# Optimization experiments

Measured on AMD Instinct MI355X. Metric: run time of the kernel, lower is better.

## Reference

```python
import jax, jax.numpy as jnp
import numpy as np

B, N, D, R = 4, 50000, 64, 500
E_PER = 62500
E = B * E_PER


def _build_edges():
    rng = np.random.default_rng(0)
    idx = np.repeat(np.arange(B), E_PER)
    vi = rng.integers(0, N, E)
    vj = rng.integers(0, N, E)
    order = np.lexsort((vj, vi, idx))
    idx, vi, vj = idx[order], vi[order], vj[order]
    rel = rng.integers(0, R, E)
    key_vi = idx.astype(np.int64) * N + vi
    _, idx_vi = np.unique(key_vi, return_inverse=True)  # sorted -> nondecreasing segment ids
    key_vj = idx.astype(np.int64) * N + vj
    _, idx_vj = np.unique(key_vj, return_inverse=True)
    all_keys = np.concatenate([key_vi, key_vj])
    uniq_all, inv = np.unique(all_keys, return_inverse=True)
    e2vi, e2vj = inv[:E], inv[E:]
    sel = np.stack([idx, vi, vj, rel, idx_vi, idx_vj, e2vi, e2vj], axis=1).astype(np.int32)
    return sel, int(idx_vi.max() + 1), int(idx_vj.max() + 1), int(len(uniq_all))


def setup_inputs() -> dict:
    sel, n_vi_seg, n_vj_seg, n_visited = _build_edges()
    key = jax.random.key(0)
    ks = jax.random.split(key, 9)
    na = jax.random.uniform(ks[0], (B, N), jnp.float32) + 1e-6
    na = na / jnp.sum(na, axis=1, keepdims=True)
    return {
        'node_attention': na,
        'selected_edges': jnp.asarray(sel),
        'edges_y': jax.random.uniform(ks[1], (E,), jnp.float32, 0.1, 1.0),
        'hidden_con': jax.random.normal(ks[2], (n_visited, D), jnp.float32) * 0.1,
        'hidden_uncon': jax.random.normal(ks[3], (1, N, D), jnp.float32) * 0.1,
        'rel_emb': jax.random.normal(ks[4], (R, D), jnp.float32) * 0.1,
        'ws': jax.random.normal(ks[5], (8, D), jnp.float32) * (1.0 / np.sqrt(8.0)),
        'b': jax.random.normal(ks[6], (D,), jnp.float32) * 0.01,
        'out_w': jax.random.normal(ks[7], (D,), jnp.float32) * 0.3,
        'out_b': jax.random.normal(ks[8], (D,), jnp.float32) * 0.01,
        'n_vi_seg': n_vi_seg,
        'n_vj_seg': n_vj_seg,
    }


def reference(node_attention, selected_edges, edges_y, hidden_con, hidden_uncon,
              rel_emb, ws, b, out_w, out_b, n_vi_seg, n_vj_seg):
    idx, vi, vj = selected_edges[:, 0], selected_edges[:, 1], selected_edges[:, 2]
    rel, idx_vi, idx_vj = selected_edges[:, 3], selected_edges[:, 4], selected_edges[:, 5]
    e2vi, e2vj = selected_edges[:, 6], selected_edges[:, 7]

    # Node2Edge gathers
    hc_vi, hc_vj = hidden_con[e2vi], hidden_con[e2vj]        # [E, D]
    hu = hidden_uncon[0]                                     # hidden_uncon has batch 1
    hu_vi, hu_vj = hu[vi], hu[vj]                            # [E, D]
    re = rel_emb[rel]                                        # [E, D]

    # F layer: interact = [[0,3],[0,2,3],[0,4],[0,2,4],[1,3],[1,2,3],[1,4],[1,2,4]]
    terms = (hc_vi * hc_vj, hc_vi * re * hc_vj, hc_vi * hu_vj, hc_vi * re * hu_vj,
             hu_vi * hc_vj, hu_vi * re * hc_vj, hu_vi * hu_vj, hu_vi * re * hu_vj)
    f = b
    for k in range(8):
        f = f + ws[k] * terms[k]
    f = jax.nn.relu(f) * out_w + out_b                       # [E, D]
    logits = jnp.sum(f, axis=1)                              # [E]

    # NeighborSoftmax at='vi' (segment softmax)
    seg_max = jax.ops.segment_max(logits, idx_vi, num_segments=n_vi_seg)
    e = jnp.exp(logits - seg_max[idx_vi])
    es = jax.ops.segment_sum(e, idx_vi, num_segments=n_vi_seg)
    transition = e / es[idx_vi]

    # attention flow
    na_e = node_attention[idx, vi]
    ta = na_e * transition * edges_y

    # Aggregate at='vj', sum, then scatter into (B, n_nodes)
    aggr = jax.ops.segment_sum(ta, idx_vj, num_segments=n_vj_seg)
    seg_idx = jax.ops.segment_max(idx, idx_vj, num_segments=n_vj_seg)
    seg_vj = jax.ops.segment_max(vj, idx_vj, num_segments=n_vj_seg)
    Bn, Nn = node_attention.shape
    new_att = jnp.zeros((Bn, Nn), node_attention.dtype).at[seg_idx, seg_vj].add(aggr)
    return new_att / jnp.sum(new_att, axis=1, keepdims=True)
```

## Files before the change

### kernel.cpp

```cpp
#include <hip/hip_runtime.h>
#include <math.h>

#define D 64

__global__ __launch_bounds__(256) void k_logits(
    const int* __restrict__ sel, const float* __restrict__ hc,
    const float* __restrict__ hu, const float* __restrict__ re,
    const float* __restrict__ wsm, const float* __restrict__ bias,
    const float* __restrict__ out_w, const float* __restrict__ out_b,
    float* __restrict__ logits, int* __restrict__ seg_start,
    float* __restrict__ out, float* __restrict__ row_sum,
    int E, int BN, int Bn)
{
    const int tid = blockIdx.x * 256 + threadIdx.x;
    const int nthreads = gridDim.x * 256;

    for (int i = tid; i < BN; i += nthreads) out[i] = 0.f;
    if (tid < Bn) row_sum[tid] = 0.f;

    const int lane = threadIdx.x & 63;
    const int g    = lane >> 4;
    const int d16  = lane & 15;

    const float4* wsm4 = (const float4*)wsm;
    float4 W[8];
    #pragma unroll
    for (int k = 0; k < 8; ++k) W[k] = wsm4[k * 16 + d16];
    const float4 Bv = ((const float4*)bias)[d16];
    const float4 Ow = ((const float4*)out_w)[d16];
    const float4 Ob = ((const float4*)out_b)[d16];
    const float* Wf  = (const float*)W;
    const float* Bvf = (const float*)&Bv;
    const float* Owf = (const float*)&Ow;
    const float* Obf = (const float*)&Ob;

    const float4* hc4 = (const float4*)hc;
    const float4* hu4 = (const float4*)hu;
    const float4* re4 = (const float4*)re;

    const int wave   = tid >> 6;
    const int nwaves = nthreads >> 6;
    const int octs   = (E + 7) >> 3;

    int q = wave;
    if (q >= octs) return;

    int ec0 = min(q * 8 + g, E - 1);
    int ec1 = min(q * 8 + 4 + g, E - 1);
    int4 sA0 = *(const int4*)(sel + (size_t)ec0 * 8);
    int4 sB0 = *(const int4*)(sel + (size_t)ec0 * 8 + 4);
    int4 sA1 = *(const int4*)(sel + (size_t)ec1 * 8);
    int4 sB1 = *(const int4*)(sel + (size_t)ec1 * 8 + 4);

    for (; q < octs; q += nwaves) {
        const int e0 = q * 8 + g;
        const int e1 = q * 8 + 4 + g;
        const bool v0 = (e0 < E);
        const bool v1 = (e1 < E);

        const float4 a0  = hc4[(size_t)sB0.z * 16 + d16];
        const float4 c0  = hc4[(size_t)sB0.w * 16 + d16];
        const float4 ui0 = hu4[(size_t)sA0.y * 16 + d16];
        const float4 uj0 = hu4[(size_t)sA0.z * 16 + d16];
        const float4 r0  = re4[(size_t)sA0.w * 16 + d16];
        const float4 a1  = hc4[(size_t)sB1.z * 16 + d16];
        const float4 c1  = hc4[(size_t)sB1.w * 16 + d16];
        const float4 ui1 = hu4[(size_t)sA1.y * 16 + d16];
        const float4 uj1 = hu4[(size_t)sA1.z * 16 + d16];
        const float4 r1  = re4[(size_t)sA1.w * 16 + d16];

        const int qn = q + nwaves;
        int4 nA0, nB0, nA1, nB1;
        const bool more = (qn < octs);
        {
            const int pe0 = more ? min(qn * 8 + g, E - 1) : ec0;
            const int pe1 = more ? min(qn * 8 + 4 + g, E - 1) : ec1;
            nA0 = *(const int4*)(sel + (size_t)pe0 * 8);
            nB0 = *(const int4*)(sel + (size_t)pe0 * 8 + 4);
            nA1 = *(const int4*)(sel + (size_t)pe1 * 8);
            nB1 = *(const int4*)(sel + (size_t)pe1 * 8 + 4);
            ec0 = pe0; ec1 = pe1;
        }

        float acc0 = 0.f, acc1 = 0.f;
        {
            const float* ap = (const float*)&a0;  const float* cp = (const float*)&c0;
            const float* up = (const float*)&ui0; const float* vp = (const float*)&uj0;
            const float* rp = (const float*)&r0;
            #pragma unroll
            for (int k4 = 0; k4 < 4; ++k4) {
                const float hcvi = ap[k4], hcvj = cp[k4], huvi = up[k4], huvj = vp[k4], rr = rp[k4];
                const float p = hcvi * hcvj, qq = hcvi * huvj, ss = huvi * hcvj, uu = huvi * huvj;
                const float w01 = fmaf(rr, Wf[1*4+k4], Wf[0*4+k4]);
                const float w23 = fmaf(rr, Wf[3*4+k4], Wf[2*4+k4]);
                const float w45 = fmaf(rr, Wf[5*4+k4], Wf[4*4+k4]);
                const float w67 = fmaf(rr, Wf[7*4+k4], Wf[6*4+k4]);
                float f = fmaf(p, w01, Bvf[k4]);
                f = fmaf(qq, w23, f);
                f = fmaf(ss, w45, f);
                f = fmaf(uu, w67, f);
                acc0 += fmaf(fmaxf(f, 0.f), Owf[k4], Obf[k4]);
            }
        }
        {
            const float* ap = (const float*)&a1;  const float* cp = (const float*)&c1;
            const float* up = (const float*)&ui1; const float* vp = (const float*)&uj1;
            const float* rp = (const float*)&r1;
            #pragma unroll
            for (int k4 = 0; k4 < 4; ++k4) {
                const float hcvi = ap[k4], hcvj = cp[k4], huvi = up[k4], huvj = vp[k4], rr = rp[k4];
                const float p = hcvi * hcvj, qq = hcvi * huvj, ss = huvi * hcvj, uu = huvi * huvj;
                const float w01 = fmaf(rr, Wf[1*4+k4], Wf[0*4+k4]);
                const float w23 = fmaf(rr, Wf[3*4+k4], Wf[2*4+k4]);
                const float w45 = fmaf(rr, Wf[5*4+k4], Wf[4*4+k4]);
                const float w67 = fmaf(rr, Wf[7*4+k4], Wf[6*4+k4]);
                float f = fmaf(p, w01, Bvf[k4]);
                f = fmaf(qq, w23, f);
                f = fmaf(ss, w45, f);
                f = fmaf(uu, w67, f);
                acc1 += fmaf(fmaxf(f, 0.f), Owf[k4], Obf[k4]);
            }
        }

        #pragma unroll
        for (int off = 8; off > 0; off >>= 1) {
            acc0 += __shfl_xor(acc0, off, 64);
            acc1 += __shfl_xor(acc1, off, 64);
        }

        const int idxvi0 = sB0.x, idxvi1 = sB1.x;
        const int srcm16 = (lane >= 16) ? (lane - 16) : lane;
        const int p0w = __shfl(idxvi0, srcm16, 64);
        const int p1w = __shfl(idxvi1, srcm16, 64);
        const int p1b = __shfl(idxvi0, 48 + d16, 64);

        if (d16 == 0) {
            if (v0) {
                logits[e0] = acc0;
                int prev;
                if (e0 == 0)     prev = -1;
                else if (g == 0) prev = sel[(size_t)(e0 - 1) * 8 + 4];
                else             prev = p0w;
                if (idxvi0 != prev) seg_start[idxvi0] = e0;
                if (e0 == E - 1) seg_start[idxvi0 + 1] = E;
            }
            if (v1) {
                logits[e1] = acc1;
                const int prev = (g == 0) ? p1b : p1w;
                if (idxvi1 != prev) seg_start[idxvi1] = e1;
                if (e1 == E - 1) seg_start[idxvi1 + 1] = E;
            }
        }

        sA0 = nA0; sB0 = nB0; sA1 = nA1; sB1 = nB1;
    }
}

__global__ __launch_bounds__(256) void k_softmax_scatter(
    const int* __restrict__ sel, const float* __restrict__ logits,
    const int* __restrict__ seg_start, const float* __restrict__ na,
    const float* __restrict__ edges_y,
    float* __restrict__ out, int E, int N)
{
    const int e = blockIdx.x * 256 + threadIdx.x;
    if (e >= E) return;

    const int4 A = *(const int4*)(sel + (size_t)e * 8);
    const int  s = sel[(size_t)e * 8 + 4];
    const int start = seg_start[s];
    const int end   = seg_start[s + 1];

    const float myl  = logits[e];
    const float na_e = na[(size_t)A.x * N + A.y];
    const float ye   = edges_y[e];

    float m = myl;
    for (int i = start; i < end; ++i) m = fmaxf(m, logits[i]);
    float sum = 0.f;
    for (int i = start; i < end; ++i) sum += __expf(logits[i] - m);

    const float ta = na_e * (__expf(myl - m) / sum) * ye;
    atomicAdd(out + (size_t)A.x * N + A.z, ta);
}

__global__ __launch_bounds__(256) void k_rowsum(
    const float4* __restrict__ out, float* __restrict__ row_sum, int N4)
{
    __shared__ float red[4];
    const int row = blockIdx.y;
    float s = 0.f;
    for (int i = blockIdx.x * 256 + threadIdx.x; i < N4; i += gridDim.x * 256) {
        const float4 v = out[(size_t)row * N4 + i];
        s += v.x + v.y + v.z + v.w;
    }
    #pragma unroll
    for (int off = 32; off > 0; off >>= 1)
        s += __shfl_xor(s, off, 64);
    if ((threadIdx.x & 63) == 0) red[threadIdx.x >> 6] = s;
    __syncthreads();
    if (threadIdx.x == 0)
        atomicAdd(row_sum + row, red[0] + red[1] + red[2] + red[3]);
}

__global__ void k_norm(float4* __restrict__ out, const float* __restrict__ row_sum, int N4) {
    const int col = blockIdx.x * blockDim.x + threadIdx.x;
    const int row = blockIdx.y;
    if (col < N4) {
        const float inv = 1.f / row_sum[row];
        const size_t i = (size_t)row * N4 + col;
        float4 v = out[i];
        v.x *= inv; v.y *= inv; v.z *= inv; v.w *= inv;
        out[i] = v;
    }
}

extern "C" void kernel_launch(void* const* d_in, const int* in_sizes, int n_in,
                              void* d_out, int out_size, void* d_ws, size_t ws_size,
                              hipStream_t stream)
{
    const float* na    = (const float*)d_in[0];
    const int*   sel   = (const int*)  d_in[1];
    const float* ey    = (const float*)d_in[2];
    const float* hc    = (const float*)d_in[3];
    const float* hu    = (const float*)d_in[4];
    const float* re    = (const float*)d_in[5];
    const float* wsm   = (const float*)d_in[6];
    const float* bias  = (const float*)d_in[7];
    const float* ow    = (const float*)d_in[8];
    const float* ob    = (const float*)d_in[9];

    float* out = (float*)d_out;

    const int E  = in_sizes[2];
    const int N  = in_sizes[4] / D;
    const int BN = in_sizes[0];
    const int Bn = BN / N;

    float* logits    = (float*)d_ws;
    int*   seg_start = (int*)  ((char*)d_ws + (size_t)E * 4);
    const size_t rs_off = (((size_t)E * 8 + 4) + 255) & ~(size_t)255;
    float* row_sum   = (float*)((char*)d_ws + rs_off);

    k_logits<<<4096, 256, 0, stream>>>(sel, hc, hu, re, wsm, bias, ow, ob,
                                       logits, seg_start, out, row_sum, E, BN, Bn);
    k_softmax_scatter<<<(E + 255) / 256, 256, 0, stream>>>(sel, logits, seg_start, na, ey,
                                                           out, E, N);
    const int N4 = N / 4;
    dim3 rgrid(16, Bn);
    k_rowsum<<<rgrid, 256, 0, stream>>>((const float4*)out, row_sum, N4);
    dim3 ngrid((N4 + 255) / 256, Bn);
    k_norm<<<ngrid, 256, 0, stream>>>((float4*)out, row_sum, N4);
}
```

Baseline: 161.7 us.

## Pack per-edge logit, scale, destination and segment into one record for the softmax pass

```diff
diff --git a/kernel.cpp b/kernel.cpp
--- a/kernel.cpp
+++ b/kernel.cpp
@@ -3,14 +3,15 @@
 
 #define D 64
 
-__global__ __launch_bounds__(256) void k_logits(
+__global__ __launch_bounds__(256, 8) void k_logits(
     const int* __restrict__ sel, const float* __restrict__ hc,
     const float* __restrict__ hu, const float* __restrict__ re,
     const float* __restrict__ wsm, const float* __restrict__ bias,
     const float* __restrict__ out_w, const float* __restrict__ out_b,
-    float* __restrict__ logits, int* __restrict__ seg_start,
+    const float* __restrict__ na, const float* __restrict__ ey,
+    int4* __restrict__ rec, int* __restrict__ seg_start,
     float* __restrict__ out, float* __restrict__ row_sum,
-    int E, int BN, int Bn)
+    int E, int N, int BN, int Bn)
 {
     const int tid = blockIdx.x * 256 + threadIdx.x;
     const int nthreads = gridDim.x * 256;
@@ -42,21 +43,18 @@
     const int nwaves = nthreads >> 6;
     const int octs   = (E + 7) >> 3;
 
-    int q = wave;
-    if (q >= octs) return;
-
-    int ec0 = min(q * 8 + g, E - 1);
-    int ec1 = min(q * 8 + 4 + g, E - 1);
-    int4 sA0 = *(const int4*)(sel + (size_t)ec0 * 8);
-    int4 sB0 = *(const int4*)(sel + (size_t)ec0 * 8 + 4);
-    int4 sA1 = *(const int4*)(sel + (size_t)ec1 * 8);
-    int4 sB1 = *(const int4*)(sel + (size_t)ec1 * 8 + 4);
-
-    for (; q < octs; q += nwaves) {
+    for (int q = wave; q < octs; q += nwaves) {
         const int e0 = q * 8 + g;
         const int e1 = q * 8 + 4 + g;
         const bool v0 = (e0 < E);
         const bool v1 = (e1 < E);
+        const int ec0 = v0 ? e0 : (E - 1);
+        const int ec1 = v1 ? e1 : (E - 1);
+
+        const int4 sA0 = *(const int4*)(sel + (size_t)ec0 * 8);
+        const int4 sB0 = *(const int4*)(sel + (size_t)ec0 * 8 + 4);
+        const int4 sA1 = *(const int4*)(sel + (size_t)ec1 * 8);
+        const int4 sB1 = *(const int4*)(sel + (size_t)ec1 * 8 + 4);
 
         const float4 a0  = hc4[(size_t)sB0.z * 16 + d16];
         const float4 c0  = hc4[(size_t)sB0.w * 16 + d16];
@@ -69,17 +67,12 @@
         const float4 uj1 = hu4[(size_t)sA1.z * 16 + d16];
         const float4 r1  = re4[(size_t)sA1.w * 16 + d16];
 
-        const int qn = q + nwaves;
-        int4 nA0, nB0, nA1, nB1;
-        const bool more = (qn < octs);
-        {
-            const int pe0 = more ? min(qn * 8 + g, E - 1) : ec0;
-            const int pe1 = more ? min(qn * 8 + 4 + g, E - 1) : ec1;
-            nA0 = *(const int4*)(sel + (size_t)pe0 * 8);
-            nB0 = *(const int4*)(sel + (size_t)pe0 * 8 + 4);
-            nA1 = *(const int4*)(sel + (size_t)pe1 * 8);
-            nB1 = *(const int4*)(sel + (size_t)pe1 * 8 + 4);
-            ec0 = pe0; ec1 = pe1;
+        float ye0 = 0.f, ye1 = 0.f, nae0 = 0.f, nae1 = 0.f;
+        if (d16 == 0) {
+            ye0  = ey[ec0];
+            ye1  = ey[ec1];
+            nae0 = na[(size_t)sA0.x * N + sA0.y];
+            nae1 = na[(size_t)sA1.x * N + sA1.y];
         }
 
         float acc0 = 0.f, acc1 = 0.f;
@@ -136,7 +129,12 @@
 
         if (d16 == 0) {
             if (v0) {
-                logits[e0] = acc0;
+                int4 rv;
+                rv.x = __float_as_int(acc0);
+                rv.y = __float_as_int(nae0 * ye0);
+                rv.z = sA0.x * N + sA0.z;
+                rv.w = idxvi0;
+                rec[e0] = rv;
                 int prev;
                 if (e0 == 0)     prev = -1;
                 else if (g == 0) prev = sel[(size_t)(e0 - 1) * 8 + 4];
@@ -145,42 +143,48 @@
                 if (e0 == E - 1) seg_start[idxvi0 + 1] = E;
             }
             if (v1) {
-                logits[e1] = acc1;
+                int4 rv;
+                rv.x = __float_as_int(acc1);
+                rv.y = __float_as_int(nae1 * ye1);
+                rv.z = sA1.x * N + sA1.z;
+                rv.w = idxvi1;
+                rec[e1] = rv;
                 const int prev = (g == 0) ? p1b : p1w;
                 if (idxvi1 != prev) seg_start[idxvi1] = e1;
                 if (e1 == E - 1) seg_start[idxvi1 + 1] = E;
             }
         }
-
-        sA0 = nA0; sB0 = nB0; sA1 = nA1; sB1 = nB1;
     }
 }
 
 __global__ __launch_bounds__(256) void k_softmax_scatter(
-    const int* __restrict__ sel, const float* __restrict__ logits,
-    const int* __restrict__ seg_start, const float* __restrict__ na,
-    const float* __restrict__ edges_y,
-    float* __restrict__ out, int E, int N)
+    const int4* __restrict__ rec, const int* __restrict__ seg_start,
+    float* __restrict__ out, int E)
 {
     const int e = blockIdx.x * 256 + threadIdx.x;
     if (e >= E) return;
 
-    const int4 A = *(const int4*)(sel + (size_t)e * 8);
-    const int  s = sel[(size_t)e * 8 + 4];
+    const int4 r = rec[e];
+    const float myl   = __int_as_float(r.x);
+    const float scale = __int_as_float(r.y);
+    const int   dst   = r.z;
+    const int   s     = r.w;
     const int start = seg_start[s];
     const int end   = seg_start[s + 1];
 
-    const float myl  = logits[e];
-    const float na_e = na[(size_t)A.x * N + A.y];
-    const float ye   = edges_y[e];
-
-    float m = myl;
-    for (int i = start; i < end; ++i) m = fmaxf(m, logits[i]);
-    float sum = 0.f;
-    for (int i = start; i < end; ++i) sum += __expf(logits[i] - m);
-
-    const float ta = na_e * (__expf(myl - m) / sum) * ye;
-    atomicAdd(out + (size_t)A.x * N + A.z, ta);
+    float ta;
+    if (end - start == 1) {
+        ta = scale;
+    } else {
+        float m = myl;
+        for (int i = start; i < end; ++i)
+            m = fmaxf(m, __int_as_float(rec[i].x));
+        float sum = 0.f;
+        for (int i = start; i < end; ++i)
+            sum += __expf(__int_as_float(rec[i].x) - m);
+        ta = scale * (__expf(myl - m) / sum);
+    }
+    atomicAdd(out + dst, ta);
 }
 
 __global__ __launch_bounds__(256) void k_rowsum(
@@ -236,15 +240,14 @@
     const int BN = in_sizes[0];
     const int Bn = BN / N;
 
-    float* logits    = (float*)d_ws;
-    int*   seg_start = (int*)  ((char*)d_ws + (size_t)E * 4);
-    const size_t rs_off = (((size_t)E * 8 + 4) + 255) & ~(size_t)255;
+    int4* rec        = (int4*)d_ws;
+    int*  seg_start  = (int*) ((char*)d_ws + (size_t)E * 16);
+    const size_t rs_off = (((size_t)E * 16 + (size_t)(E + 1) * 4) + 255) & ~(size_t)255;
     float* row_sum   = (float*)((char*)d_ws + rs_off);
 
-    k_logits<<<4096, 256, 0, stream>>>(sel, hc, hu, re, wsm, bias, ow, ob,
-                                       logits, seg_start, out, row_sum, E, BN, Bn);
-    k_softmax_scatter<<<(E + 255) / 256, 256, 0, stream>>>(sel, logits, seg_start, na, ey,
-                                                           out, E, N);
+    k_logits<<<2048, 256, 0, stream>>>(sel, hc, hu, re, wsm, bias, ow, ob, na, ey,
+                                       rec, seg_start, out, row_sum, E, N, BN, Bn);
+    k_softmax_scatter<<<(E + 255) / 256, 256, 0, stream>>>(rec, seg_start, out, E);
     const int N4 = N / 4;
     dim3 rgrid(16, Bn);
     k_rowsum<<<rgrid, 256, 0, stream>>>((const float4*)out, row_sum, N4);
```

After: 435.7 us. 2.69x slower.
